# Kernel tuning notes

Hardware: AMD Instinct MI355X
Metric: run time of the kernel (lower is better)

Reference implementation:

```python
import jax, jax.numpy as jnp
import numpy as np

B, S, D, H = 4, 2048, 1024, 16
HD = D // H


def setup_inputs() -> dict:
    key = jax.random.key(0)
    ks = jax.random.split(key, 12)
    inp = {
        "query": jax.random.normal(ks[0], (B, S, D), jnp.float32),
        "key": jax.random.normal(ks[1], (B, S, D), jnp.float32),
        "value": jax.random.normal(ks[2], (B, S, D), jnp.float32),
        "mask": jnp.tril(jnp.ones((S, S), jnp.int32)),  # causal mask
        "Wq": jax.random.normal(ks[3], (D, D), jnp.float32) / np.sqrt(D),
        "bq": jax.random.normal(ks[4], (D,), jnp.float32) * 0.02,
        "Wk": jax.random.normal(ks[5], (D, D), jnp.float32) / np.sqrt(D),
        "bk": jax.random.normal(ks[6], (D,), jnp.float32) * 0.02,
        "Wv": jax.random.normal(ks[7], (D, D), jnp.float32) / np.sqrt(D),
        "bv": jax.random.normal(ks[8], (D,), jnp.float32) * 0.02,
        "Wo": jax.random.normal(ks[9], (D, D), jnp.float32) / np.sqrt(D),
        "bo": jax.random.normal(ks[10], (D,), jnp.float32) * 0.02,
    }
    return inp


def reference(query, key, value, mask, Wq, bq, Wk, bk, Wv, bv, Wo, bo):
    # Linear projections (torch nn.Linear: y = x @ W.T + b)
    q = query @ Wq.T + bq
    k = key @ Wk.T + bk
    v = value @ Wv.T + bv
    # split heads: [B, S, D] -> [B, H, S, HD]
    q = q.reshape(B, S, H, HD).transpose(0, 2, 1, 3)
    k = k.reshape(B, S, H, HD).transpose(0, 2, 1, 3)
    v = v.reshape(B, S, H, HD).transpose(0, 2, 1, 3)
    # scaled dot-product attention with full [B,H,S,S] scores (faithful to source)
    scores = jnp.einsum("bhqd,bhkd->bhqk", q, k) / jnp.sqrt(jnp.float32(HD))
    scores = jnp.where(mask == 0, -jnp.inf, scores)
    attn = jax.nn.softmax(scores, axis=-1)
    out = jnp.einsum("bhqk,bhkd->bhqd", attn, v)
    # merge heads and output projection (dropout rate = 0.0 -> identity)
    out = out.transpose(0, 2, 1, 3).reshape(B, S, D)
    return out @ Wo.T + bo
```

## Files before the change

kernel.cpp:

```cpp
#include <hip/hip_runtime.h>

typedef __bf16 bf16x8 __attribute__((ext_vector_type(8)));
typedef __bf16 bf16x2 __attribute__((ext_vector_type(2)));
typedef float f32x4 __attribute__((ext_vector_type(4)));
typedef float f32x16 __attribute__((ext_vector_type(16)));
typedef unsigned short ushort;

__device__ __forceinline__ int4 cvt8(float4 a, float4 b) {
  bf16x8 v;
  v[0] = (__bf16)a.x; v[1] = (__bf16)a.y; v[2] = (__bf16)a.z; v[3] = (__bf16)a.w;
  v[4] = (__bf16)b.x; v[5] = (__bf16)b.y; v[6] = (__bf16)b.z; v[7] = (__bf16)b.w;
  return __builtin_bit_cast(int4, v);
}

__device__ __forceinline__ void gld16(const void* g, void* l) {
  __builtin_amdgcn_global_load_lds(
      (const __attribute__((address_space(1))) void*)g,
      (__attribute__((address_space(3))) void*)l, 16, 0, 0);
}

__device__ __forceinline__ unsigned pkbf(float a, float b) {
  bf16x2 v;
  v[0] = (__bf16)a;
  v[1] = (__bf16)b;
  return __builtin_bit_cast(unsigned, v);
}

#if __has_builtin(__builtin_amdgcn_permlane32_swap)
typedef unsigned u32x2 __attribute__((ext_vector_type(2)));
__device__ __forceinline__ void plswap(unsigned& a, unsigned& b, int hi) {
  (void)hi;
  u32x2 r = __builtin_amdgcn_permlane32_swap(a, b, false, false);
  a = r[0]; b = r[1];
}
#else
__device__ __forceinline__ void plswap(unsigned& a, unsigned& b, int hi) {
  const unsigned pa = (unsigned)__shfl_xor((int)a, 32);
  const unsigned pb = (unsigned)__shfl_xor((int)b, 32);
  const unsigned x = hi ? pb : a;
  const unsigned y = hi ? b : pa;
  a = x; b = y;
}
#endif

__device__ __forceinline__ f32x16 mfma32(bf16x8 a, bf16x8 b, f32x16 c) {
  return __builtin_amdgcn_mfma_f32_32x32x16_bf16(a, b, c, 0, 0, 0);
}

__global__ __launch_bounds__(256) void cvt4_k(const float* __restrict__ i0,
                                              const float* __restrict__ i1,
                                              const float* __restrict__ i2,
                                              const float* __restrict__ i3,
                                              ushort* __restrict__ o, int n8) {
  const int z = blockIdx.y;
  const float* in = (z == 0) ? i0 : (z == 1) ? i1 : (z == 2) ? i2 : i3;
  ushort* out = o + (size_t)z * 1024 * 1024;
  int i = blockIdx.x * 256 + threadIdx.x;
  if (i >= n8) return;
  const float4* p = (const float4*)in + (size_t)i * 2;
  *(int4*)(out + (size_t)i * 8) = cvt8(p[0], p[1]);
}

template <int AMODE, int OMODE>
__global__ __launch_bounds__(256) void gemm_k(const void* __restrict__ A,
                                              const ushort* __restrict__ W,
                                              const float* __restrict__ bias,
                                              void* __restrict__ Out,
                                              float oscale) {
  constexpr int K = 1024;
  __shared__ __align__(16) char lds_all[4][16384];
#define lAbuf(b) (lds_all[(b)])
#define lBbuf(b) (lds_all[2 + (b)])
  const int t = threadIdx.x;
  const int l = t & 63;
  const int w = t >> 6;
  const int wr = w >> 1, wc = w & 1;
  const int bid = blockIdx.x;
  const int xcd = bid & 7, j = bid >> 3;
  const int m0 = (xcd * 8 + (j >> 3)) * 128;
  const int n0 = (j & 7) * 128;
  const int srow = l >> 3;
  const int scol = ((l & 7) ^ srow) << 3;
  const int ar = t >> 3;
  const int ac = (t & 7) * 8;
  const float* Abase = (const float*)A + (size_t)(m0 + ar) * K + ac;
  const int adst = ar * 128 + ((ac * 2) ^ ((ar & 7) << 4));
  float4 a0, a1, a2, a3, a4, a5, a6, a7;

#define LOAD_A(k0)                                         \
  do {                                                     \
    const float* ap = Abase + (k0);                        \
    a0 = *(const float4*)(ap);                             \
    a1 = *(const float4*)(ap + 4);                         \
    a2 = *(const float4*)(ap + 32 * K);                    \
    a3 = *(const float4*)(ap + 32 * K + 4);                \
    a4 = *(const float4*)(ap + 64 * K);                    \
    a5 = *(const float4*)(ap + 64 * K + 4);                \
    a6 = *(const float4*)(ap + 96 * K);                    \
    a7 = *(const float4*)(ap + 96 * K + 4);                \
  } while (0)
#define CVT_WRITE(b)                                       \
  do {                                                     \
    *(int4*)(lAbuf(b) + adst) = cvt8(a0, a1);              \
    *(int4*)(lAbuf(b) + adst + 32 * 128) = cvt8(a2, a3);   \
    *(int4*)(lAbuf(b) + adst + 64 * 128) = cvt8(a4, a5);   \
    *(int4*)(lAbuf(b) + adst + 96 * 128) = cvt8(a6, a7);   \
  } while (0)
#define GLD_A(k0, b)                                                        \
  do {                                                                      \
    _Pragma("unroll") for (int i = 0; i < 4; ++i) {                         \
      const int chunk = w * 4 + i;                                          \
      gld16((const ushort*)A + (size_t)(m0 + chunk * 8 + srow) * K + (k0) + \
                scol,                                                       \
            lAbuf(b) + chunk * 1024);                                       \
    }                                                                       \
  } while (0)
#define GLD_W(k0, b)                                                         \
  do {                                                                       \
    _Pragma("unroll") for (int i = 0; i < 4; ++i) {                          \
      const int chunk = w * 4 + i;                                           \
      gld16(W + (size_t)(n0 + chunk * 8 + srow) * K + (k0) + scol,           \
            lBbuf(b) + chunk * 1024);                                        \
    }                                                                        \
  } while (0)

  f32x4 acc[4][4];
#pragma unroll
  for (int i = 0; i < 4; ++i)
#pragma unroll
    for (int j2 = 0; j2 < 4; ++j2) acc[i][j2] = (f32x4){0.f, 0.f, 0.f, 0.f};

  if constexpr (AMODE == 0) {
    LOAD_A(0);
    CVT_WRITE(0);
  } else {
    GLD_A(0, 0);
  }
  GLD_W(0, 0);
  __syncthreads();

  int buf = 0;
  for (int k0 = 0; k0 < K; k0 += 64) {
    const int nk = k0 + 64;
    if (nk < K) {
      if constexpr (AMODE == 0) LOAD_A(nk);
      else GLD_A(nk, buf ^ 1);
      GLD_W(nk, buf ^ 1);
    }
#pragma unroll
    for (int ks = 0; ks < 2; ++ks) {
      const int kb = ks * 64 + ((l >> 4) << 4);
      bf16x8 af[4], bfv[4];
#pragma unroll
      for (int i = 0; i < 4; ++i) {
        const int row = wr * 64 + i * 16 + (l & 15);
        af[i] = *(const bf16x8*)(lAbuf(buf) + row * 128 + (kb ^ ((row & 7) << 4)));
      }
#pragma unroll
      for (int j2 = 0; j2 < 4; ++j2) {
        const int row = wc * 64 + j2 * 16 + (l & 15);
        bfv[j2] = *(const bf16x8*)(lBbuf(buf) + row * 128 + (kb ^ ((row & 7) << 4)));
      }
#pragma unroll
      for (int i = 0; i < 4; ++i)
#pragma unroll
        for (int j2 = 0; j2 < 4; ++j2)
          acc[i][j2] = __builtin_amdgcn_mfma_f32_16x16x32_bf16(af[i], bfv[j2],
                                                               acc[i][j2], 0, 0, 0);
    }
    if constexpr (AMODE == 0) {
      if (nk < K) CVT_WRITE(buf ^ 1);
    }
    __syncthreads();
    buf ^= 1;
  }
#undef LOAD_A
#undef CVT_WRITE
#undef GLD_A
#undef GLD_W

  if constexpr (OMODE == 3) {
    ushort* T = (ushort*)lds_all;
#pragma unroll
    for (int i = 0; i < 4; ++i)
#pragma unroll
      for (int j2 = 0; j2 < 4; ++j2) {
        const int gn_l = wc * 64 + j2 * 16 + (l & 15);
        const int gm_l = wr * 64 + i * 16 + ((l >> 4) << 2);
        const float bb = bias[n0 + gn_l];
        ushort4 u;
        u.x = __builtin_bit_cast(ushort, (__bf16)((acc[i][j2][0] + bb) * oscale));
        u.y = __builtin_bit_cast(ushort, (__bf16)((acc[i][j2][1] + bb) * oscale));
        u.z = __builtin_bit_cast(ushort, (__bf16)((acc[i][j2][2] + bb) * oscale));
        u.w = __builtin_bit_cast(ushort, (__bf16)((acc[i][j2][3] + bb) * oscale));
        *(ushort4*)(T + gn_l * 136 + gm_l) = u;
      }
    __syncthreads();
    const int gn_r = t >> 1, half = t & 1;
    const int hd_g = n0 + gn_r;
    const int hh = hd_g >> 6, hd = hd_g & 63;
    const int bb2 = m0 >> 11;
    const int s0 = (m0 & 2047) + half * 64;
    ushort* obase = (ushort*)Out +
                    (((size_t)(bb2 * 16 + hh) << 6) + hd) * 2048 + s0;
#pragma unroll
    for (int k2 = 0; k2 < 8; ++k2) {
      const int4 vd = *(const int4*)((const char*)T + (size_t)gn_r * 272 +
                                     half * 128 + k2 * 16);
      *(int4*)(obase + k2 * 8) = vd;
    }
  } else {
#pragma unroll
    for (int i = 0; i < 4; ++i)
#pragma unroll
      for (int j2 = 0; j2 < 4; ++j2)
#pragma unroll
        for (int rg = 0; rg < 4; ++rg) {
          const int gm = m0 + wr * 64 + i * 16 + ((l >> 4) << 2) + rg;
          const int gn = n0 + wc * 64 + j2 * 16 + (l & 15);
          const float v = (acc[i][j2][rg] + bias[gn]) * oscale;
          if constexpr (OMODE == 0) {
            const int b = gm >> 11, s = gm & 2047, h = gn >> 6, hd = gn & 63;
            ((ushort*)Out)[((((size_t)(b * 16 + h)) * 2048 + s) << 6) + hd] =
                __builtin_bit_cast(ushort, (__bf16)v);
          } else {
            ((float*)Out)[(size_t)gm * 1024 + gn] = v;
          }
        }
  }
#undef lAbuf
#undef lBbuf
}

template <int OMODE, int AM>
__global__ __launch_bounds__(256) void gemmF_k(const void* __restrict__ A,
                                               const float* __restrict__ Wf,
                                               const float* __restrict__ bias,
                                               void* __restrict__ Out,
                                               float oscale) {
  constexpr int K = 1024;
  __shared__ __align__(16) char lA[128 * 128];
  __shared__ __align__(16) char lB[128 * 128];
  const int t = threadIdx.x;
  const int l = t & 63;
  const int w = t >> 6;
  const int wr = w >> 1, wc = w & 1;
  const int m0 = blockIdx.x * 128;
  const int n0 = blockIdx.y * 128;
  f32x4 acc[4][4];
#pragma unroll
  for (int i = 0; i < 4; ++i)
#pragma unroll
    for (int j = 0; j < 4; ++j) acc[i][j] = (f32x4){0.f, 0.f, 0.f, 0.f};
  for (int k0 = 0; k0 < K; k0 += 64) {
#pragma unroll
    for (int qq = 0; qq < 4; ++qq) {
      const int L = t * 8 + qq * 2048;
      const int r = L >> 6, c = L & 63;
      const int dst = r * 128 + ((c * 2) ^ ((r & 7) << 4));
      if constexpr (AM == 0) {
        const float* s0 = (const float*)A + (size_t)(m0 + r) * K + k0 + c;
        *(int4*)(lA + dst) = cvt8(*(const float4*)s0, *(const float4*)(s0 + 4));
      } else {
        *(int4*)(lA + dst) =
            *(const int4*)((const ushort*)A + (size_t)(m0 + r) * K + k0 + c);
      }
      const float* s1 = Wf + (size_t)(n0 + r) * K + k0 + c;
      *(int4*)(lB + dst) = cvt8(*(const float4*)s1, *(const float4*)(s1 + 4));
    }
    __syncthreads();
#pragma unroll
    for (int ks = 0; ks < 2; ++ks) {
      const int kb = ks * 64 + ((l >> 4) << 4);
      bf16x8 af[4], bfv[4];
#pragma unroll
      for (int i = 0; i < 4; ++i) {
        const int row = wr * 64 + i * 16 + (l & 15);
        af[i] = *(const bf16x8*)(lA + row * 128 + (kb ^ ((row & 7) << 4)));
      }
#pragma unroll
      for (int j = 0; j < 4; ++j) {
        const int row = wc * 64 + j * 16 + (l & 15);
        bfv[j] = *(const bf16x8*)(lB + row * 128 + (kb ^ ((row & 7) << 4)));
      }
#pragma unroll
      for (int i = 0; i < 4; ++i)
#pragma unroll
        for (int j = 0; j < 4; ++j)
          acc[i][j] = __builtin_amdgcn_mfma_f32_16x16x32_bf16(af[i], bfv[j],
                                                              acc[i][j], 0, 0, 0);
    }
    __syncthreads();
  }
#pragma unroll
  for (int i = 0; i < 4; ++i)
#pragma unroll
    for (int j = 0; j < 4; ++j)
#pragma unroll
      for (int rg = 0; rg < 4; ++rg) {
        const int gm = m0 + wr * 64 + i * 16 + ((l >> 4) << 2) + rg;
        const int gn = n0 + wc * 64 + j * 16 + (l & 15);
        const float v = (acc[i][j][rg] + bias[gn]) * oscale;
        if constexpr (OMODE == 0) {
          const int b = gm >> 11, s = gm & 2047, h = gn >> 6, hd = gn & 63;
          ((ushort*)Out)[((((size_t)(b * 16 + h)) * 2048 + s) << 6) + hd] =
              __builtin_bit_cast(ushort, (__bf16)v);
        } else if constexpr (OMODE == 1) {
          const int b = gm >> 11, s = gm & 2047, h = gn >> 6, hd = gn & 63;
          ((ushort*)Out)[((((size_t)(b * 16 + h)) << 6) + hd) * 2048 + s] =
              __builtin_bit_cast(ushort, (__bf16)v);
        } else {
          ((float*)Out)[(size_t)gm * 1024 + gn] = v;
        }
      }
}

__global__ __launch_bounds__(256, 6) void attn_k(const ushort* __restrict__ qh,
                                                 const ushort* __restrict__ kh,
                                                 const ushort* __restrict__ vth,
                                                 ushort* __restrict__ out) {
  const int bh = blockIdx.x;
  const int qt = gridDim.y - 1 - blockIdx.y;
  const int q0 = qt * 128;
  const int t = threadIdx.x, l = t & 63, wv = t >> 6;
  const int lq = l & 31, hi = l >> 5;
  __shared__ __align__(16) char lk[2][64 * 128];
  __shared__ __align__(16) char lv[2][64 * 128];

  const int qrow = q0 + wv * 32 + lq;
  bf16x8 qf0, qf1, qf2, qf3;
  {
    const ushort* qp = qh + ((size_t)bh * 2048 + qrow) * 64 + hi * 8;
    qf0 = *(const bf16x8*)(qp);
    qf1 = *(const bf16x8*)(qp + 16);
    qf2 = *(const bf16x8*)(qp + 32);
    qf3 = *(const bf16x8*)(qp + 48);
  }

  const int r0 = t >> 3;
  const int c0 = (t & 7) * 8;
  const ushort* kbase = kh + (size_t)bh * 2048 * 64 + (size_t)r0 * 64 + c0;
  const ushort* vbase = vth + (size_t)bh * 64 * 2048 + (size_t)r0 * 2048 + c0;
  const int dst0 = r0 * 128 + ((c0 * 2) ^ ((r0 & 7) << 4));

  int4 ka, kb2, va, vb2;
#define LOAD_TILE(kv0)                                            \
  do {                                                            \
    ka  = *(const int4*)(kbase + (size_t)(kv0) * 64);             \
    kb2 = *(const int4*)(kbase + (size_t)(kv0) * 64 + 32 * 64);   \
    va  = *(const int4*)(vbase + (kv0));                          \
    vb2 = *(const int4*)(vbase + (kv0) + 32 * 2048);              \
  } while (0)
#define WRITE_TILE(buf)                                           \
  do {                                                            \
    *(int4*)(lk[buf] + dst0) = ka;                                \
    *(int4*)(lk[buf] + dst0 + 32 * 128) = kb2;                    \
    *(int4*)(lv[buf] + dst0) = va;                                \
    *(int4*)(lv[buf] + dst0 + 32 * 128) = vb2;                    \
  } while (0)

  LOAD_TILE(0);
  WRITE_TILE(0);

  float l_r = 0.f;
  f32x16 acco[2];
#pragma unroll
  for (int dt = 0; dt < 2; ++dt)
#pragma unroll
    for (int r = 0; r < 16; ++r) acco[dt][r] = 0.f;

  const int nt = 2 * qt + 2;
  int cur = 0;
#pragma unroll 1
  for (int ti = 0; ti < nt; ++ti) {
    __syncthreads();
    if (ti + 1 < nt) LOAD_TILE((ti + 1) << 6);

#pragma unroll
    for (int s = 0; s < 2; ++s) {
      const int kvs = (ti << 6) + s * 32;
      if (kvs > q0 + wv * 32 + 31) continue;

      f32x16 p;
#pragma unroll
      for (int r = 0; r < 16; ++r) p[r] = 0.f;
      __builtin_amdgcn_s_setprio(1);
#pragma unroll
      for (int kd = 0; kd < 4; ++kd) {
        const int row = s * 32 + lq;
        const bf16x8 kf = *(const bf16x8*)(
            lk[cur] + row * 128 + ((kd * 32 + hi * 16) ^ ((row & 7) << 4)));
        const bf16x8 qf = (kd == 0) ? qf0 : (kd == 1) ? qf1 : (kd == 2) ? qf2 : qf3;
        p = mfma32(kf, qf, p);
      }
      __builtin_amdgcn_s_setprio(0);
      if (kvs + 31 > q0 + wv * 32) {
#pragma unroll
        for (int r = 0; r < 16; ++r) {
          const int kv = kvs + (r & 3) + 8 * (r >> 2) + 4 * hi;
          if (kv > qrow) p[r] = -1e30f;
        }
      }
#pragma unroll
      for (int r = 0; r < 16; ++r) p[r] = __builtin_amdgcn_exp2f(p[r] - 8.0f);
      float sr[8];
#pragma unroll
      for (int r = 0; r < 8; ++r) sr[r] = p[r] + p[r + 8];
#pragma unroll
      for (int r = 0; r < 4; ++r) sr[r] = sr[r] + sr[r + 4];
      float rs = (sr[0] + sr[1]) + (sr[2] + sr[3]);
      rs += __shfl_xor(rs, 32);
      l_r += rs;
      unsigned W0a = pkbf(p[0], p[1]),   W0b = pkbf(p[2], p[3]);
      unsigned W1a = pkbf(p[4], p[5]),   W1b = pkbf(p[6], p[7]);
      unsigned W2a = pkbf(p[8], p[9]),   W2b = pkbf(p[10], p[11]);
      unsigned W3a = pkbf(p[12], p[13]), W3b = pkbf(p[14], p[15]);
#pragma unroll
      for (int ks = 0; ks < 2; ++ks) {
        unsigned a0u = ks ? W2a : W0a;
        unsigned a1u = ks ? W2b : W0b;
        unsigned b0u = ks ? W3a : W1a;
        unsigned b1u = ks ? W3b : W1b;
        plswap(a0u, b0u, hi);
        plswap(a1u, b1u, hi);
        const uint4 pw = {a0u, a1u, b0u, b1u};
        const bf16x8 pf = __builtin_bit_cast(bf16x8, pw);
        __builtin_amdgcn_s_setprio(1);
#pragma unroll
        for (int dt = 0; dt < 2; ++dt) {
          const int row = dt * 32 + lq;
          const bf16x8 vf = *(const bf16x8*)(
              lv[cur] + row * 128 +
              ((s * 64 + ks * 32 + hi * 16) ^ ((row & 7) << 4)));
          acco[dt] = mfma32(vf, pf, acco[dt]);
        }
        __builtin_amdgcn_s_setprio(0);
      }
    }
    if (ti + 1 < nt) WRITE_TILE(cur ^ 1);
    cur ^= 1;
  }
#undef LOAD_TILE
#undef WRITE_TILE
  const int b = bh >> 4, h = bh & 15;
  const float inv = __builtin_amdgcn_rcpf(l_r);
  ushort* orow = out + ((size_t)(b * 2048 + qrow)) * 1024 + h * 64;
#pragma unroll
  for (int dt = 0; dt < 2; ++dt)
#pragma unroll
    for (int g = 0; g < 4; ++g) {
      ushort4 st;
      st.x = __builtin_bit_cast(ushort, (__bf16)(acco[dt][4 * g + 0] * inv));
      st.y = __builtin_bit_cast(ushort, (__bf16)(acco[dt][4 * g + 1] * inv));
      st.z = __builtin_bit_cast(ushort, (__bf16)(acco[dt][4 * g + 2] * inv));
      st.w = __builtin_bit_cast(ushort, (__bf16)(acco[dt][4 * g + 3] * inv));
      *(ushort4*)(orow + dt * 32 + g * 8 + hi * 4) = st;
    }
}

extern "C" void kernel_launch(void* const* d_in, const int* in_sizes, int n_in,
                              void* d_out, int out_size, void* d_ws, size_t ws_size,
                              hipStream_t stream) {
  (void)in_sizes; (void)n_in; (void)out_size;
  const float* query = (const float*)d_in[0];
  const float* key = (const float*)d_in[1];
  const float* value = (const float*)d_in[2];
  const float* Wq = (const float*)d_in[4];
  const float* bq = (const float*)d_in[5];
  const float* Wk = (const float*)d_in[6];
  const float* bk = (const float*)d_in[7];
  const float* Wv = (const float*)d_in[8];
  const float* bv = (const float*)d_in[9];
  const float* Wo = (const float*)d_in[10];
  const float* bo = (const float*)d_in[11];

  char* ws = (char*)d_ws;
  const size_t SZA = (size_t)8192 * 1024 * 2;
  const size_t SZW = (size_t)1024 * 1024 * 2;
  ushort* qh = (ushort*)(ws + 0 * SZA);
  ushort* kh = (ushort*)(ws + 1 * SZA);
  ushort* vt = (ushort*)(ws + 2 * SZA);
  ushort* ao = (ushort*)(ws + 3 * SZA);
  dim3 bb(256), gg(512), ga(64, 16), ba(256);
  const float QS = 0.125f * 1.44269504088896f;

  if (ws_size >= 4 * SZA + 4 * SZW) {
    ushort* wq = (ushort*)(ws + 4 * SZA);
    ushort* wk = (ushort*)(ws + 4 * SZA + 1 * SZW);
    ushort* wv = (ushort*)(ws + 4 * SZA + 2 * SZW);
    ushort* wo = (ushort*)(ws + 4 * SZA + 3 * SZW);
    const int n8w = 1024 * 1024 / 8;
    hipLaunchKernelGGL(cvt4_k, dim3(n8w / 256, 4), bb, 0, stream, Wq, Wk, Wv, Wo, wq, n8w);
    hipLaunchKernelGGL((gemm_k<0, 0>), gg, bb, 0, stream, (const void*)query, wq, bq, (void*)qh, QS);
    hipLaunchKernelGGL((gemm_k<0, 0>), gg, bb, 0, stream, (const void*)key, wk, bk, (void*)kh, 1.0f);
    hipLaunchKernelGGL((gemm_k<0, 3>), gg, bb, 0, stream, (const void*)value, wv, bv, (void*)vt, 1.0f);
    hipLaunchKernelGGL(attn_k, ga, ba, 0, stream, qh, kh, vt, ao);
    hipLaunchKernelGGL((gemm_k<1, 2>), gg, bb, 0, stream, (const void*)ao, wo, bo, d_out, 1.0f);
  } else {
    hipLaunchKernelGGL((gemmF_k<0, 0>), dim3(64, 8), bb, 0, stream, (const void*)query, Wq, bq, (void*)qh, QS);
    hipLaunchKernelGGL((gemmF_k<0, 0>), dim3(64, 8), bb, 0, stream, (const void*)key, Wk, bk, (void*)kh, 1.0f);
    hipLaunchKernelGGL((gemmF_k<1, 0>), dim3(64, 8), bb, 0, stream, (const void*)value, Wv, bv, (void*)vt, 1.0f);
    hipLaunchKernelGGL(attn_k, ga, ba, 0, stream, qh, kh, vt, ao);
    hipLaunchKernelGGL((gemmF_k<2, 1>), dim3(64, 8), bb, 0, stream, (const void*)ao, Wo, bo, d_out, 1.0f);
  }
}
```

Before: 169.7 us.

## Split long causal attention query tiles across two blocks and combine partials

The eight longest causal query tiles (qt 8..15) are each split into two KV-range halves processed by separate blocks. Unnormalized fp32 accumulators and row sums go to workspace, and a new combine kernel sums them and normalizes. The grid grows from 16 to 24 y-blocks to even out the causal load imbalance and the tail. In exchange it adds an extra launch and fp32 partial traffic, and it needs a larger workspace, otherwise it falls back to the old path. The combine relies on both halves using the same fixed max-free exp2 scaling, so plain summation is valid.

Result: slower. 177.2 us (+4.5%).

```diff
diff --git a/kernel.cpp b/kernel.cpp
--- a/kernel.cpp
+++ b/kernel.cpp
@@ -315,12 +315,33 @@
       }
 }
 
+template <int SPLIT>
 __global__ __launch_bounds__(256, 6) void attn_k(const ushort* __restrict__ qh,
                                                  const ushort* __restrict__ kh,
                                                  const ushort* __restrict__ vth,
-                                                 ushort* __restrict__ out) {
+                                                 ushort* __restrict__ out,
+                                                 float* __restrict__ pacc,
+                                                 float* __restrict__ pl) {
   const int bh = blockIdx.x;
-  const int qt = gridDim.y - 1 - blockIdx.y;
+  int qt, t0, t1, half = 0;
+  if constexpr (SPLIT) {
+    const int y = blockIdx.y;
+    if (y < 16) {
+      qt = 15 - (y >> 1);
+      half = y & 1;
+      const int len = qt + 1;
+      t0 = half * len;
+      t1 = t0 + len;
+    } else {
+      qt = 23 - y;
+      t0 = 0;
+      t1 = 2 * qt + 2;
+    }
+  } else {
+    qt = gridDim.y - 1 - blockIdx.y;
+    t0 = 0;
+    t1 = 2 * qt + 2;
+  }
   const int q0 = qt * 128;
   const int t = threadIdx.x, l = t & 63, wv = t >> 6;
   const int lq = l & 31, hi = l >> 5;
@@ -359,7 +380,7 @@
     *(int4*)(lv[buf] + dst0 + 32 * 128) = vb2;                    \
   } while (0)
 
-  LOAD_TILE(0);
+  LOAD_TILE(t0 << 6);
   WRITE_TILE(0);
 
   float l_r = 0.f;
@@ -369,12 +390,11 @@
 #pragma unroll
     for (int r = 0; r < 16; ++r) acco[dt][r] = 0.f;
 
-  const int nt = 2 * qt + 2;
   int cur = 0;
 #pragma unroll 1
-  for (int ti = 0; ti < nt; ++ti) {
+  for (int ti = t0; ti < t1; ++ti) {
     __syncthreads();
-    if (ti + 1 < nt) LOAD_TILE((ti + 1) << 6);
+    if (ti + 1 < t1) LOAD_TILE((ti + 1) << 6);
 
 #pragma unroll
     for (int s = 0; s < 2; ++s) {
@@ -437,11 +457,30 @@
         __builtin_amdgcn_s_setprio(0);
       }
     }
-    if (ti + 1 < nt) WRITE_TILE(cur ^ 1);
+    if (ti + 1 < t1) WRITE_TILE(cur ^ 1);
     cur ^= 1;
   }
 #undef LOAD_TILE
 #undef WRITE_TILE
+  if constexpr (SPLIT) {
+    if (blockIdx.y < 16) {
+      const int rowi = (bh << 10) | (qrow & 1023);
+      float* ab = pacc + (size_t)half * 4194304 + ((size_t)rowi << 6);
+#pragma unroll
+      for (int dt = 0; dt < 2; ++dt)
+#pragma unroll
+        for (int g = 0; g < 4; ++g) {
+          float4 st;
+          st.x = acco[dt][4 * g + 0];
+          st.y = acco[dt][4 * g + 1];
+          st.z = acco[dt][4 * g + 2];
+          st.w = acco[dt][4 * g + 3];
+          *(float4*)(ab + dt * 32 + g * 8 + hi * 4) = st;
+        }
+      pl[half * 65536 + rowi] = l_r;
+      return;
+    }
+  }
   const int b = bh >> 4, h = bh & 15;
   const float inv = __builtin_amdgcn_rcpf(l_r);
   ushort* orow = out + ((size_t)(b * 2048 + qrow)) * 1024 + h * 64;
@@ -456,6 +495,35 @@
       st.w = __builtin_bit_cast(ushort, (__bf16)(acco[dt][4 * g + 3] * inv));
       *(ushort4*)(orow + dt * 32 + g * 8 + hi * 4) = st;
     }
+}
+
+__global__ __launch_bounds__(256) void combine_k(const float* __restrict__ pacc,
+                                                 const float* __restrict__ pl,
+                                                 ushort* __restrict__ out) {
+  const int i = blockIdx.x * 256 + threadIdx.x;
+  const int rowi = i >> 3;
+  const int dblk = (i & 7) * 8;
+  const float* A0 = pacc + ((size_t)rowi << 6) + dblk;
+  const float* A1 = A0 + 4194304;
+  const float lsum = pl[rowi] + pl[rowi + 65536];
+  const float inv = __builtin_amdgcn_rcpf(lsum);
+  const float4 x0 = *(const float4*)A0;
+  const float4 x1 = *(const float4*)(A0 + 4);
+  const float4 y0 = *(const float4*)A1;
+  const float4 y1 = *(const float4*)(A1 + 4);
+  bf16x8 v;
+  v[0] = (__bf16)((x0.x + y0.x) * inv);
+  v[1] = (__bf16)((x0.y + y0.y) * inv);
+  v[2] = (__bf16)((x0.z + y0.z) * inv);
+  v[3] = (__bf16)((x0.w + y0.w) * inv);
+  v[4] = (__bf16)((x1.x + y1.x) * inv);
+  v[5] = (__bf16)((x1.y + y1.y) * inv);
+  v[6] = (__bf16)((x1.z + y1.z) * inv);
+  v[7] = (__bf16)((x1.w + y1.w) * inv);
+  const int bh = rowi >> 10, q = (rowi & 1023) + 1024;
+  const int b = bh >> 4, h = bh & 15;
+  *(int4*)(out + ((size_t)(b * 2048 + q)) * 1024 + h * 64 + dblk) =
+      __builtin_bit_cast(int4, v);
 }
 
 extern "C" void kernel_launch(void* const* d_in, const int* in_sizes, int n_in,
@@ -477,14 +545,17 @@
   char* ws = (char*)d_ws;
   const size_t SZA = (size_t)8192 * 1024 * 2;
   const size_t SZW = (size_t)1024 * 1024 * 2;
+  const size_t BASE = 4 * SZA + 4 * SZW;
+  const size_t SZP = (size_t)2 * 4194304 * 4;
+  const size_t SZL = (size_t)2 * 65536 * 4;
   ushort* qh = (ushort*)(ws + 0 * SZA);
   ushort* kh = (ushort*)(ws + 1 * SZA);
   ushort* vt = (ushort*)(ws + 2 * SZA);
   ushort* ao = (ushort*)(ws + 3 * SZA);
-  dim3 bb(256), gg(512), ga(64, 16), ba(256);
+  dim3 bb(256), gg(512), ba(256);
   const float QS = 0.125f * 1.44269504088896f;
 
-  if (ws_size >= 4 * SZA + 4 * SZW) {
+  if (ws_size >= BASE) {
     ushort* wq = (ushort*)(ws + 4 * SZA);
     ushort* wk = (ushort*)(ws + 4 * SZA + 1 * SZW);
     ushort* wv = (ushort*)(ws + 4 * SZA + 2 * SZW);
@@ -494,13 +565,22 @@
     hipLaunchKernelGGL((gemm_k<0, 0>), gg, bb, 0, stream, (const void*)query, wq, bq, (void*)qh, QS);
     hipLaunchKernelGGL((gemm_k<0, 0>), gg, bb, 0, stream, (const void*)key, wk, bk, (void*)kh, 1.0f);
     hipLaunchKernelGGL((gemm_k<0, 3>), gg, bb, 0, stream, (const void*)value, wv, bv, (void*)vt, 1.0f);
-    hipLaunchKernelGGL(attn_k, ga, ba, 0, stream, qh, kh, vt, ao);
+    if (ws_size >= BASE + SZP + SZL) {
+      float* pacc = (float*)(ws + BASE);
+      float* pl = (float*)(ws + BASE + SZP);
+      hipLaunchKernelGGL((attn_k<1>), dim3(64, 24), ba, 0, stream, qh, kh, vt, ao, pacc, pl);
+      hipLaunchKernelGGL(combine_k, dim3(2048), bb, 0, stream, pacc, pl, ao);
+    } else {
+      hipLaunchKernelGGL((attn_k<0>), dim3(64, 16), ba, 0, stream, qh, kh, vt, ao,
+                         (float*)nullptr, (float*)nullptr);
+    }
     hipLaunchKernelGGL((gemm_k<1, 2>), gg, bb, 0, stream, (const void*)ao, wo, bo, d_out, 1.0f);
   } else {
     hipLaunchKernelGGL((gemmF_k<0, 0>), dim3(64, 8), bb, 0, stream, (const void*)query, Wq, bq, (void*)qh, QS);
     hipLaunchKernelGGL((gemmF_k<0, 0>), dim3(64, 8), bb, 0, stream, (const void*)key, Wk, bk, (void*)kh, 1.0f);
     hipLaunchKernelGGL((gemmF_k<1, 0>), dim3(64, 8), bb, 0, stream, (const void*)value, Wv, bv, (void*)vt, 1.0f);
-    hipLaunchKernelGGL(attn_k, ga, ba, 0, stream, qh, kh, vt, ao);
+    hipLaunchKernelGGL((attn_k<0>), dim3(64, 16), ba, 0, stream, qh, kh, vt, ao,
+                       (float*)nullptr, (float*)nullptr);
     hipLaunchKernelGGL((gemmF_k<2, 1>), dim3(64, 8), bb, 0, stream, (const void*)ao, Wo, bo, d_out, 1.0f);
   }
 }
```
